# Kernel tuning notes

Measured on AMD Instinct MI355X. Metric: run time of the kernel, lower is better.

Reference implementation:

```python
import jax, jax.numpy as jnp
import numpy as np

V = 32000; DM = 1024; DS = 16; NL = 2; DC = 4; EXP = 2
DI = EXP * DM          # 2048 inner dim
DTR = DM // 16         # 64 dt_rank = ceil(d_model/16)
B = 2; L = 1024


def setup_inputs() -> dict:
    key = jax.random.key(0)
    ks = jax.random.split(key, 9)
    s = lambda k, shp, sc: jax.random.normal(k, shp, jnp.float32) * sc
    return {
        "input_ids": jax.random.randint(ks[0], (B, L), 0, V),
        "embed": s(ks[1], (V, DM), 0.02),
        "in_proj": s(ks[2], (NL, DM, 2 * DI), DM ** -0.5),
        "conv_w": s(ks[3], (NL, DI, DC), 0.2),
        "conv_b": jnp.zeros((NL, DI), jnp.float32),
        "x_proj": s(ks[4], (NL, DI, DTR + 2 * DS), DI ** -0.5),
        "dt_proj_w": s(ks[5], (NL, DTR, DI), DTR ** -0.5),
        "dt_proj_b": jnp.full((NL, DI), -4.6, jnp.float32),  # softplus ~= 0.01
        "A_log": jnp.tile(jnp.log(jnp.arange(1, DS + 1, dtype=jnp.float32))[None, None, :], (NL, DI, 1)),
        "D": jnp.ones((NL, DI), jnp.float32),
        "out_proj": s(ks[6], (NL, DI, DM), DI ** -0.5),
        "ln_g": jnp.ones((DM,), jnp.float32),
        "ln_b": jnp.zeros((DM,), jnp.float32),
        "head": s(ks[7], (DM, V), DM ** -0.5),
    }


def _silu(x):
    return x * jax.nn.sigmoid(x)


def _mamba_layer(x, Wi, cw, cb, Wx, Wdt, bdt, A_log, Dv, Wo):
    # x: [B,L,DM]
    xz = x @ Wi                                   # [B,L,2*DI]
    xin, z = jnp.split(xz, 2, axis=-1)
    # causal depthwise conv1d, kernel DC
    xp = jnp.pad(xin, ((0, 0), (DC - 1, 0), (0, 0)))
    conv = sum(xp[:, k:k + x.shape[1], :] * cw[:, k] for k in range(DC)) + cb
    u = _silu(conv)                               # [B,L,DI]
    dbc = u @ Wx                                  # [B,L,DTR+2*DS]
    dt = dbc[..., :DTR]
    Bm = dbc[..., DTR:DTR + DS]                   # [B,L,DS]
    Cm = dbc[..., DTR + DS:]                      # [B,L,DS]
    delta = jax.nn.softplus(dt @ Wdt + bdt)       # [B,L,DI]
    A = -jnp.exp(A_log)                           # [DI,DS]
    dA = jnp.exp(delta[..., None] * A)            # [B,L,DI,DS]
    dBu = (delta * u)[..., None] * Bm[:, :, None, :]

    def comb(c1, c2):
        a1, b1 = c1
        a2, b2 = c2
        return a1 * a2, a2 * b1 + b2

    _, h = jax.lax.associative_scan(comb, (dA, dBu), axis=1)  # [B,L,DI,DS]
    y = jnp.einsum('bldn,bln->bld', h, Cm) + u * Dv
    y = y * _silu(z)
    return y @ Wo


def reference(input_ids, embed, in_proj, conv_w, conv_b, x_proj, dt_proj_w,
              dt_proj_b, A_log, D, out_proj, ln_g, ln_b, head):
    x = embed[input_ids]                          # [B,L,DM]
    for i in range(NL):
        x = _mamba_layer(x, in_proj[i], conv_w[i], conv_b[i], x_proj[i],
                         dt_proj_w[i], dt_proj_b[i], A_log[i], D[i], out_proj[i])
    mu = jnp.mean(x, -1, keepdims=True)
    var = jnp.var(x, -1, keepdims=True)
    x = (x - mu) * jax.lax.rsqrt(var + 1e-5) * ln_g + ln_b
    return x @ head                               # [B,L,V]
```

## Files before the change

kernel.cpp:

```cpp
#include <hip/hip_runtime.h>

typedef unsigned short u16;
typedef __attribute__((ext_vector_type(8))) short bf16x8;
typedef __attribute__((ext_vector_type(4))) float f32x4;
typedef __attribute__((ext_vector_type(4))) u16 u16x4;

#define DEV static __device__ __forceinline__

DEV u16 f2bf(float f) {
  union { float f; unsigned u; } v; v.f = f;
  unsigned r = (v.u + 0x7fffu + ((v.u >> 16) & 1u)) >> 16;
  return (u16)r;
}

DEV void gload_lds16(const void* g, void* l) {
  __builtin_amdgcn_global_load_lds(
      (const __attribute__((address_space(1))) unsigned int*)g,
      (__attribute__((address_space(3))) unsigned int*)l, 16, 0, 0);
}

#define STGH(buf, mat, half, P, kt) { \
    const int r_ = (half) * 128 + sr0; \
    gload_lds16((P) + (size_t)r_ * K + (kt) + scs, &lds[buf][mat][r_][sc8]); \
    gload_lds16((P) + (size_t)(r_ + 64) * K + (kt) + scs, &lds[buf][mat][r_ + 64][sc8]); }
#define LDB(buf) _Pragma("unroll") for (int n = 0; n < 4; ++n) { \
    const int row = wn * 64 + n * 16 + lr; \
    _Pragma("unroll") for (int kk = 0; kk < 2; ++kk) \
      bfr[n][kk] = *(const bf16x8*)&lds[buf][1][row][(((kk << 2) | lq) ^ (row & 7)) << 3]; }
#define LDA(buf, p) _Pragma("unroll") for (int mi = 0; mi < 2; ++mi) { \
    const int row = wm * 128 + ((p) * 2 + mi) * 16 + lr; \
    _Pragma("unroll") for (int kk = 0; kk < 2; ++kk) \
      af[mi][kk] = *(const bf16x8*)&lds[buf][0][row][(((kk << 2) | lq) ^ (row & 7)) << 3]; }
#define MM(p) __builtin_amdgcn_s_setprio(1); \
  _Pragma("unroll") for (int kk = 0; kk < 2; ++kk) \
  _Pragma("unroll") for (int mi = 0; mi < 2; ++mi) \
  _Pragma("unroll") for (int n = 0; n < 4; ++n) \
    acc[(p) * 2 + mi][n] = __builtin_amdgcn_mfma_f32_16x16x32_bf16(af[mi][kk], bfr[n][kk], acc[(p) * 2 + mi][n], 0, 0, 0); \
  __builtin_amdgcn_s_setprio(0);
#define BAR() { __builtin_amdgcn_s_barrier(); asm volatile("" ::: "memory"); }
#define WLG() { asm volatile("s_waitcnt lgkmcnt(0)" ::: "memory"); __builtin_amdgcn_sched_barrier(0); }
#define VMC(n) asm volatile("s_waitcnt vmcnt(" #n ")" ::: "memory")

__global__ __launch_bounds__(512, 1)
void gemm256(const u16* __restrict__ A, const u16* __restrict__ BT,
             float* __restrict__ C, int M, int N, int K) {
  __shared__ u16 lds[2][2][256][64];
  const int t = threadIdx.x;
  const int l = t & 63;
  const int w = t >> 6;
  const int wm = w >> 2;
  const int wn = w & 3;
  const int lr = l & 15, lq = l >> 4;

  const int gn = N >> 8;
  const int nwg = gn << 3;
  const int orig = blockIdx.y * 8 + blockIdx.x;
  const int q = nwg >> 3;
  const int swz = (orig & 7) * q + (orig >> 3);
  const int bx = swz & 7;
  const int by = swz >> 3;

  const u16* Ap = A + (size_t)bx * 256 * K;
  const u16* Bp = BT + (size_t)by * 256 * K;
  const int sr0 = t >> 3;
  const int sc8 = (t & 7) << 3;
  const int scs = (((t & 7) ^ (sr0 & 7)) << 3);

  f32x4 acc[8][4];
#pragma unroll
  for (int m = 0; m < 8; ++m)
#pragma unroll
    for (int n = 0; n < 4; ++n) acc[m][n] = (f32x4){0.f, 0.f, 0.f, 0.f};

  const int NI = K >> 7;
  STGH(0, 1, 0, Bp, 0) STGH(0, 1, 1, Bp, 0)
  STGH(0, 0, 0, Ap, 0) STGH(0, 0, 1, Ap, 0)
  STGH(1, 1, 0, Bp, 64) STGH(1, 1, 1, Bp, 64)
  VMC(4);
  BAR();

  for (int ip = 0; ip < NI; ++ip) {
    const int k0 = ip << 7;
    const bool m2 = (k0 + 128) < K;
    const bool m3 = (k0 + 192) < K;
    bf16x8 bfr[4][2], af[2][2];
    LDB(0) LDA(0, 0)
    STGH(1, 0, 0, Ap, k0 + 64)
    BAR(); WLG(); MM(0) BAR();
    LDA(0, 1)
    STGH(1, 0, 1, Ap, k0 + 64)
    BAR(); WLG(); MM(1) BAR();
    LDA(0, 2)
    if (m2) STGH(0, 1, 0, Bp, k0 + 128)
    BAR(); WLG(); MM(2) BAR();
    LDA(0, 3)
    if (m2) STGH(0, 1, 1, Bp, k0 + 128)
    BAR(); WLG(); MM(3)
    if (m2) { VMC(4); } else { VMC(0); }
    BAR();
    LDB(1) LDA(1, 0)
    if (m2) STGH(0, 0, 0, Ap, k0 + 128)
    BAR(); WLG(); MM(0) BAR();
    LDA(1, 1)
    if (m2) STGH(0, 0, 1, Ap, k0 + 128)
    BAR(); WLG(); MM(1) BAR();
    LDA(1, 2)
    if (m3) STGH(1, 1, 0, Bp, k0 + 192)
    BAR(); WLG(); MM(2) BAR();
    LDA(1, 3)
    if (m3) STGH(1, 1, 1, Bp, k0 + 192)
    BAR(); WLG(); MM(3)
    if (m3) { VMC(4); } else { VMC(0); }
    BAR();
  }

  const int lg4 = lq * 4;
#pragma unroll
  for (int m = 0; m < 8; ++m) {
    const int grow0 = bx * 256 + wm * 128 + m * 16 + lg4;
#pragma unroll
    for (int n = 0; n < 4; ++n) {
      const int gcol = by * 256 + wn * 64 + n * 16 + lr;
#pragma unroll
      for (int r = 0; r < 4; ++r) {
        const size_t idx = (size_t)(grow0 + r) * N + gcol;
        C[idx] = acc[m][n][r];
      }
    }
  }
}
#undef STGH
#undef LDB
#undef LDA
#undef MM
#undef BAR
#undef WLG
#undef VMC

template<int EPI>
__global__ __launch_bounds__(256)
void gemm_bt(const u16* __restrict__ A, const u16* __restrict__ BT,
             float* __restrict__ C, const float* __restrict__ bias,
             int M, int N, int K) {
  __shared__ u16 As[128][64];
  __shared__ u16 Bs[128][64];
  const int t = threadIdx.x;
  const int l = t & 63;
  const int w = t >> 6;
  const int wr = (w >> 1) * 64;
  const int wc = (w & 1) * 64;

  const int nwg = gridDim.x * gridDim.y;
  const int orig = blockIdx.y * gridDim.x + blockIdx.x;
  const int swz = (orig & 7) * (nwg >> 3) + (orig >> 3);
  const int bx = swz & 15;
  const int by = swz >> 4;

  const size_t aoff = (size_t)bx * 128 * K;
  const size_t boff = (size_t)by * 128 * K;
  const int r0 = t >> 3;
  const int c0s = (((t & 7) ^ (r0 & 7)) << 3);
  const int c0l = (t & 7) << 3;
  const int lr = l & 15;
  const int lq = l >> 4;

  f32x4 acc[4][4];
#pragma unroll
  for (int i = 0; i < 4; ++i)
#pragma unroll
    for (int j = 0; j < 4; ++j) acc[i][j] = (f32x4){0.f, 0.f, 0.f, 0.f};

  for (int kt = 0; kt < K; kt += 64) {
    __syncthreads();
#pragma unroll
    for (int i = 0; i < 4; ++i) {
      const int r = r0 + i * 32;
      gload_lds16(A + aoff + (size_t)r * K + kt + c0s, &As[r][c0l]);
      gload_lds16(BT + boff + (size_t)r * K + kt + c0s, &Bs[r][c0l]);
    }
    __syncthreads();
#pragma unroll
    for (int kk = 0; kk < 2; ++kk) {
      bf16x8 af[4], bfr[4];
#pragma unroll
      for (int i = 0; i < 4; ++i) {
        const int row = wr + i * 16 + lr;
        af[i] = *(const bf16x8*)&As[row][(((kk << 2) | lq) ^ (row & 7)) << 3];
      }
#pragma unroll
      for (int j = 0; j < 4; ++j) {
        const int row = wc + j * 16 + lr;
        bfr[j] = *(const bf16x8*)&Bs[row][(((kk << 2) | lq) ^ (row & 7)) << 3];
      }
#pragma unroll
      for (int i = 0; i < 4; ++i)
#pragma unroll
        for (int j = 0; j < 4; ++j)
          acc[i][j] = __builtin_amdgcn_mfma_f32_16x16x32_bf16(af[i], bfr[j], acc[i][j], 0, 0, 0);
    }
  }

  const int lg4 = lq * 4;
#pragma unroll
  for (int i = 0; i < 4; ++i) {
    const int grow0 = bx * 128 + wr + i * 16 + lg4;
#pragma unroll
    for (int j = 0; j < 4; ++j) {
      const int gcol = by * 128 + wc + j * 16 + lr;
      float bv = 0.f;
      if (EPI == 1) bv = bias[gcol];
#pragma unroll
      for (int r = 0; r < 4; ++r) {
        float v = acc[i][j][r];
        if (EPI == 1) {
          v += bv;
          v = fmaxf(v, 0.f) + log1pf(expf(-fabsf(v)));
        }
        C[(size_t)(grow0 + r) * N + gcol] = v;
      }
    }
  }
}

__global__ __launch_bounds__(256)
void xproj_split(const u16* __restrict__ A, const u16* __restrict__ BT,
                 float* __restrict__ P) {
  __shared__ u16 As[128][64];
  __shared__ u16 Bs[128][64];
  const int t = threadIdx.x;
  const int l = t & 63;
  const int w = t >> 6;
  const int wr = (w >> 1) * 64;
  const int wc = (w & 1) * 64;
  const int bx = blockIdx.x;
  const int ch = blockIdx.y;
  const int kb = ch * 256;

  const size_t aoff = (size_t)bx * 128 * 2048 + kb;
  const int r0 = t >> 3;
  const int c0s = (((t & 7) ^ (r0 & 7)) << 3);
  const int c0l = (t & 7) << 3;
  const int lr = l & 15;
  const int lq = l >> 4;

  f32x4 acc[4][4];
#pragma unroll
  for (int i = 0; i < 4; ++i)
#pragma unroll
    for (int j = 0; j < 4; ++j) acc[i][j] = (f32x4){0.f, 0.f, 0.f, 0.f};

  for (int kt = 0; kt < 256; kt += 64) {
    __syncthreads();
#pragma unroll
    for (int i = 0; i < 4; ++i) {
      const int r = r0 + i * 32;
      gload_lds16(A + aoff + (size_t)r * 2048 + kt + c0s, &As[r][c0l]);
      gload_lds16(BT + (size_t)r * 2048 + kb + kt + c0s, &Bs[r][c0l]);
    }
    __syncthreads();
#pragma unroll
    for (int kk = 0; kk < 2; ++kk) {
      bf16x8 af[4], bfr[4];
#pragma unroll
      for (int i = 0; i < 4; ++i) {
        const int row = wr + i * 16 + lr;
        af[i] = *(const bf16x8*)&As[row][(((kk << 2) | lq) ^ (row & 7)) << 3];
      }
#pragma unroll
      for (int j = 0; j < 4; ++j) {
        const int row = wc + j * 16 + lr;
        bfr[j] = *(const bf16x8*)&Bs[row][(((kk << 2) | lq) ^ (row & 7)) << 3];
      }
#pragma unroll
      for (int i = 0; i < 4; ++i)
#pragma unroll
        for (int j = 0; j < 4; ++j)
          acc[i][j] = __builtin_amdgcn_mfma_f32_16x16x32_bf16(af[i], bfr[j], acc[i][j], 0, 0, 0);
    }
  }

  float* __restrict__ Pc = P + (size_t)ch * 262144;
  const int lg4 = lq * 4;
#pragma unroll
  for (int i = 0; i < 4; ++i) {
    const int grow0 = bx * 128 + wr + i * 16 + lg4;
#pragma unroll
    for (int j = 0; j < 4; ++j) {
      const int gcol = wc + j * 16 + lr;
#pragma unroll
      for (int r = 0; r < 4; ++r)
        Pc[(size_t)(grow0 + r) * 128 + gcol] = acc[i][j][r];
    }
  }
}

__global__ __launch_bounds__(256)
void merge_x(const float* __restrict__ P, float* __restrict__ dbc,
             u16* __restrict__ dtbf) {
  const int idx = blockIdx.x * 256 + threadIdx.x;
  float s = 0.f;
#pragma unroll
  for (int ch = 0; ch < 8; ++ch) s += P[(size_t)ch * 262144 + idx];
  dbc[idx] = s;
  const int c = idx & 127, r = idx >> 7;
  if (c < 64) dtbf[r * 64 + c] = f2bf(s);
}

__global__ __launch_bounds__(256)
void outproj_split(const u16* __restrict__ A, const u16* __restrict__ BT,
                   float* __restrict__ P) {
  __shared__ u16 As[128][64];
  __shared__ u16 Bs[128][64];
  const int t = threadIdx.x;
  const int l = t & 63;
  const int w = t >> 6;
  const int wr = (w >> 1) * 64;
  const int wc = (w & 1) * 64;
  const int bx = blockIdx.x;
  const int byn = blockIdx.y & 7;
  const int ch = blockIdx.y >> 3;
  const int kb = ch * 1024;

  const size_t aoff = (size_t)bx * 128 * 2048 + kb;
  const size_t boff = (size_t)byn * 128 * 2048 + kb;
  const int r0 = t >> 3;
  const int c0s = (((t & 7) ^ (r0 & 7)) << 3);
  const int c0l = (t & 7) << 3;
  const int lr = l & 15;
  const int lq = l >> 4;

  f32x4 acc[4][4];
#pragma unroll
  for (int i = 0; i < 4; ++i)
#pragma unroll
    for (int j = 0; j < 4; ++j) acc[i][j] = (f32x4){0.f, 0.f, 0.f, 0.f};

  for (int kt = 0; kt < 1024; kt += 64) {
    __syncthreads();
#pragma unroll
    for (int i = 0; i < 4; ++i) {
      const int r = r0 + i * 32;
      gload_lds16(A + aoff + (size_t)r * 2048 + kt + c0s, &As[r][c0l]);
      gload_lds16(BT + boff + (size_t)r * 2048 + kt + c0s, &Bs[r][c0l]);
    }
    __syncthreads();
#pragma unroll
    for (int kk = 0; kk < 2; ++kk) {
      bf16x8 af[4], bfr[4];
#pragma unroll
      for (int i = 0; i < 4; ++i) {
        const int row = wr + i * 16 + lr;
        af[i] = *(const bf16x8*)&As[row][(((kk << 2) | lq) ^ (row & 7)) << 3];
      }
#pragma unroll
      for (int j = 0; j < 4; ++j) {
        const int row = wc + j * 16 + lr;
        bfr[j] = *(const bf16x8*)&Bs[row][(((kk << 2) | lq) ^ (row & 7)) << 3];
      }
#pragma unroll
      for (int i = 0; i < 4; ++i)
#pragma unroll
        for (int j = 0; j < 4; ++j)
          acc[i][j] = __builtin_amdgcn_mfma_f32_16x16x32_bf16(af[i], bfr[j], acc[i][j], 0, 0, 0);
    }
  }

  float* __restrict__ Pc = P + (size_t)ch * 2097152;
  const int lg4 = lq * 4;
#pragma unroll
  for (int i = 0; i < 4; ++i) {
    const int grow0 = bx * 128 + wr + i * 16 + lg4;
#pragma unroll
    for (int j = 0; j < 4; ++j) {
      const int gcol = byn * 128 + wc + j * 16 + lr;
#pragma unroll
      for (int r = 0; r < 4; ++r)
        Pc[(size_t)(grow0 + r) * 1024 + gcol] = acc[i][j][r];
    }
  }
}

__global__ __launch_bounds__(256)
void merge_o1(const float* __restrict__ P, u16* __restrict__ xbf) {
  const int i4 = (blockIdx.x * 256 + threadIdx.x) * 4;
  const float4 a = *(const float4*)(P + i4);
  const float4 b = *(const float4*)(P + 2097152 + i4);
  u16x4 o = { f2bf(a.x + b.x), f2bf(a.y + b.y), f2bf(a.z + b.z), f2bf(a.w + b.w) };
  *(u16x4*)(xbf + i4) = o;
}

__global__ __launch_bounds__(256)
void merge_o2_ln(const float* __restrict__ P, const float* __restrict__ g,
                 const float* __restrict__ bta, u16* __restrict__ out) {
  __shared__ float red1[4], red2[4];
  const int r = blockIdx.x;
  const int tid = threadIdx.x;
  const int lane = tid & 63, wid = tid >> 6;
  const int c4 = tid * 4;
  const float4 a = *(const float4*)(P + (size_t)r * 1024 + c4);
  const float4 b = *(const float4*)(P + 2097152 + (size_t)r * 1024 + c4);
  float4 v = { a.x + b.x, a.y + b.y, a.z + b.z, a.w + b.w };
  float s = v.x + v.y + v.z + v.w;
#pragma unroll
  for (int m = 1; m < 64; m <<= 1) s += __shfl_xor(s, m, 64);
  if (lane == 0) red1[wid] = s;
  __syncthreads();
  const float mu = (red1[0] + red1[1] + red1[2] + red1[3]) * (1.f / 1024.f);
  const float d0 = v.x - mu, d1 = v.y - mu, d2 = v.z - mu, d3 = v.w - mu;
  float q = d0 * d0 + d1 * d1 + d2 * d2 + d3 * d3;
#pragma unroll
  for (int m = 1; m < 64; m <<= 1) q += __shfl_xor(q, m, 64);
  if (lane == 0) red2[wid] = q;
  __syncthreads();
  const float rs = rsqrtf((red2[0] + red2[1] + red2[2] + red2[3]) * (1.f / 1024.f) + 1e-5f);
  const float4 gv = *(const float4*)(g + c4);
  const float4 bv = *(const float4*)(bta + c4);
  u16x4 o = { f2bf(d0 * rs * gv.x + bv.x), f2bf(d1 * rs * gv.y + bv.y),
              f2bf(d2 * rs * gv.z + bv.z), f2bf(d3 * rs * gv.w + bv.w) };
  *(u16x4*)(out + (size_t)r * 1024 + c4) = o;
}

struct TBatch {
  const float* src[10];
  u16* dst[10];
  int K[10], N[10], tx[10];
  int start[11];
  int njobs;
  const int* ids;
};

__global__ __launch_bounds__(256)
void transpose_batch(TBatch tb) {
  const int tile = blockIdx.x;
  int j = 0;
  while (j + 1 < tb.njobs && tile >= tb.start[j + 1]) ++j;
  const int lt = tile - tb.start[j];

  if (tb.tx[j] < 0) {
    const int c = threadIdx.x * 4;
    const int id = tb.ids[lt];
    const float4 v = *(const float4*)(tb.src[j] + (size_t)id * 1024 + c);
    u16x4 o = { f2bf(v.x), f2bf(v.y), f2bf(v.z), f2bf(v.w) };
    *(u16x4*)(tb.dst[j] + (size_t)lt * 1024 + c) = o;
    return;
  }

  const int K = tb.K[j];
  const int N = tb.N[j];
  const int kb = (lt % tb.tx[j]) * 32;
  const int nb = (lt / tb.tx[j]) * 32;
  const float* __restrict__ in = tb.src[j];
  u16* __restrict__ out = tb.dst[j];

  __shared__ float tile_s[32][33];
  const int tx = threadIdx.x & 31;
  const int ty = threadIdx.x >> 5;
#pragma unroll
  for (int s = 0; s < 4; ++s) {
    const int k = kb + ty + s * 8;
    const int n = nb + tx;
    tile_s[ty + s * 8][tx] = (n < N) ? __builtin_nontemporal_load(in + (size_t)k * N + n) : 0.f;
  }
  __syncthreads();
#pragma unroll
  for (int s = 0; s < 4; ++s) {
    const int n = nb + ty + s * 8;
    const int k = kb + tx;
    out[(size_t)n * K + k] = f2bf(tile_s[tx][ty + s * 8]);
  }
}

__global__ __launch_bounds__(256)
void conv_silu4(const float* __restrict__ xz, const float* __restrict__ cw,
                const float* __restrict__ cb, float* __restrict__ u,
                u16* __restrict__ ubf) {
  const int i4 = (blockIdx.x * 256 + threadIdx.x) * 4;
  const int d = i4 & 2047;
  const int r = i4 >> 11;
  const int t = r & 1023;
  float4 acc = *(const float4*)(cb + d);
  const float4 w0 = *(const float4*)(cw + (d + 0) * 4);
  const float4 w1 = *(const float4*)(cw + (d + 1) * 4);
  const float4 w2 = *(const float4*)(cw + (d + 2) * 4);
  const float4 w3 = *(const float4*)(cw + (d + 3) * 4);
#pragma unroll
  for (int k = 0; k < 4; ++k) {
    const int tt = t - 3 + k;
    if (tt >= 0) {
      const float4 x4 = *(const float4*)(xz + (size_t)(r - 3 + k) * 4096 + d);
      acc.x = fmaf(x4.x, ((const float*)&w0)[k], acc.x);
      acc.y = fmaf(x4.y, ((const float*)&w1)[k], acc.y);
      acc.z = fmaf(x4.z, ((const float*)&w2)[k], acc.z);
      acc.w = fmaf(x4.w, ((const float*)&w3)[k], acc.w);
    }
  }
  const float4 s = { acc.x / (1.f + __expf(-acc.x)), acc.y / (1.f + __expf(-acc.y)),
                     acc.z / (1.f + __expf(-acc.z)), acc.w / (1.f + __expf(-acc.w)) };
  *(float4*)(u + i4) = s;
  u16x4 o = { f2bf(s.x), f2bf(s.y), f2bf(s.z), f2bf(s.w) };
  *(u16x4*)(ubf + i4) = o;
}

__global__ __launch_bounds__(256)
void scan_pass1(const float* __restrict__ delta, const float* __restrict__ u,
                const float* __restrict__ dbc, const float* __restrict__ A_log,
                float* __restrict__ Pb, float* __restrict__ Qb) {
  const int blk = blockIdx.x;
  const int ch = blk & 15;
  if (ch == 15) return;
  const int dt = (blk >> 4) & 7;
  const int b = blk >> 7;
  const int d = dt * 256 + threadIdx.x;

  float Ac[16], h[16], P[16];
#pragma unroll
  for (int n = 0; n < 16; ++n) {
    Ac[n] = -expf(A_log[d * 16 + n]) * 1.44269504f;
    h[n] = 0.f;
    P[n] = 1.f;
  }
  const int r0 = b * 1024 + ch * 64;
  for (int j = 0; j < 64; ++j) {
    const size_t r = r0 + j;
    const float dlt = delta[r * 2048 + d];
    const float uu = u[r * 2048 + d];
    const float du = dlt * uu;
    const float4 B0 = *(const float4*)(dbc + r * 128 + 64);
    const float4 B1 = *(const float4*)(dbc + r * 128 + 68);
    const float4 B2 = *(const float4*)(dbc + r * 128 + 72);
    const float4 B3 = *(const float4*)(dbc + r * 128 + 76);
    const float Bv[16] = { B0.x, B0.y, B0.z, B0.w, B1.x, B1.y, B1.z, B1.w,
                           B2.x, B2.y, B2.z, B2.w, B3.x, B3.y, B3.z, B3.w };
#pragma unroll
    for (int n = 0; n < 16; ++n) {
      const float da = exp2f(dlt * Ac[n]);
      P[n] *= da;
      h[n] = fmaf(da, h[n], du * Bv[n]);
    }
  }
  const size_t o = ((size_t)ch * 4096 + b * 2048 + d) * 16;
#pragma unroll
  for (int n = 0; n < 16; ++n) { Pb[o + n] = P[n]; Qb[o + n] = h[n]; }
}

__global__ __launch_bounds__(256)
void scan_pass2(const float* __restrict__ delta, const float* __restrict__ u,
                const float* __restrict__ dbc, const float* __restrict__ xz,
                const float* __restrict__ A_log, const float* __restrict__ Dp,
                const float* __restrict__ Pb, const float* __restrict__ Qb,
                u16* __restrict__ ybf) {
  const int blk = blockIdx.x;
  const int ch = blk & 15;
  const int dt = (blk >> 4) & 7;
  const int b = blk >> 7;
  const int d = dt * 256 + threadIdx.x;

  float Ac[16], h[16];
#pragma unroll
  for (int n = 0; n < 16; ++n) {
    Ac[n] = -expf(A_log[d * 16 + n]) * 1.44269504f;
    h[n] = 0.f;
  }
  const float Dd = Dp[d];

  for (int cc = 0; cc < ch; ++cc) {
    const size_t o = ((size_t)cc * 4096 + b * 2048 + d) * 16;
#pragma unroll
    for (int n = 0; n < 16; ++n)
      h[n] = fmaf(Pb[o + n], h[n], Qb[o + n]);
  }

  const int r0 = b * 1024 + ch * 64;
  for (int j = 0; j < 64; ++j) {
    const size_t r = r0 + j;
    const float dlt = delta[r * 2048 + d];
    const float uu = u[r * 2048 + d];
    const float zz = xz[r * 4096 + 2048 + d];
    const float du = dlt * uu;
    const float4 B0 = *(const float4*)(dbc + r * 128 + 64);
    const float4 B1 = *(const float4*)(dbc + r * 128 + 68);
    const float4 B2 = *(const float4*)(dbc + r * 128 + 72);
    const float4 B3 = *(const float4*)(dbc + r * 128 + 76);
    const float4 C0 = *(const float4*)(dbc + r * 128 + 80);
    const float4 C1 = *(const float4*)(dbc + r * 128 + 84);
    const float4 C2 = *(const float4*)(dbc + r * 128 + 88);
    const float4 C3 = *(const float4*)(dbc + r * 128 + 92);
    const float Bv[16] = { B0.x, B0.y, B0.z, B0.w, B1.x, B1.y, B1.z, B1.w,
                           B2.x, B2.y, B2.z, B2.w, B3.x, B3.y, B3.z, B3.w };
    const float Cv[16] = { C0.x, C0.y, C0.z, C0.w, C1.x, C1.y, C1.z, C1.w,
                           C2.x, C2.y, C2.z, C2.w, C3.x, C3.y, C3.z, C3.w };
    float p0 = 0.f, p1 = 0.f, p2 = 0.f, p3 = 0.f;
#pragma unroll
    for (int n = 0; n < 16; n += 4) {
      float da;
      da = exp2f(dlt * Ac[n + 0]); h[n + 0] = fmaf(da, h[n + 0], du * Bv[n + 0]); p0 = fmaf(h[n + 0], Cv[n + 0], p0);
      da = exp2f(dlt * Ac[n + 1]); h[n + 1] = fmaf(da, h[n + 1], du * Bv[n + 1]); p1 = fmaf(h[n + 1], Cv[n + 1], p1);
      da = exp2f(dlt * Ac[n + 2]); h[n + 2] = fmaf(da, h[n + 2], du * Bv[n + 2]); p2 = fmaf(h[n + 2], Cv[n + 2], p2);
      da = exp2f(dlt * Ac[n + 3]); h[n + 3] = fmaf(da, h[n + 3], du * Bv[n + 3]); p3 = fmaf(h[n + 3], Cv[n + 3], p3);
    }
    const float p = (p0 + p1) + (p2 + p3);
    const float yv = (p + uu * Dd) * (zz / (1.f + __expf(-zz)));
    ybf[r * 2048 + d] = f2bf(yv);
  }
}

extern "C" void kernel_launch(void* const* d_in, const int* in_sizes, int n_in,
                              void* d_out, int out_size, void* d_ws, size_t ws_size,
                              hipStream_t stream) {
  (void)in_sizes; (void)n_in; (void)out_size; (void)ws_size;
  const int*   ids      = (const int*)d_in[0];
  const float* embed    = (const float*)d_in[1];
  const float* in_proj  = (const float*)d_in[2];
  const float* conv_w   = (const float*)d_in[3];
  const float* conv_b   = (const float*)d_in[4];
  const float* x_proj   = (const float*)d_in[5];
  const float* dt_w     = (const float*)d_in[6];
  const float* dt_b     = (const float*)d_in[7];
  const float* A_log    = (const float*)d_in[8];
  const float* Dp       = (const float*)d_in[9];
  const float* out_proj = (const float*)d_in[10];
  const float* ln_g     = (const float*)d_in[11];
  const float* ln_bta   = (const float*)d_in[12];
  const float* head     = (const float*)d_in[13];

  float* fout = (float*)d_out;
  float* xz   = fout;
  float* ubuf = fout + 8388608;
  float* dbuf = fout + 12582912;
  float* dbc  = fout + 16777216;
  float* Pb   = fout + 17039360;
  float* Qb   = fout + 18087936;
  float* xpp  = fout + 19136512;
  float* opp  = fout + 21233664;

  u16* tail = (u16*)(fout + 26000000);
  u16* WiT[2]  = { tail,                tail + 4194304 };
  u16* WxT[2]  = { tail + 8388608,      tail + 8650752 };
  u16* WdtT[2] = { tail + 8912896,      tail + 9043968 };
  u16* WoT[2]  = { tail + 9175040,      tail + 11272192 };

  char* wp = (char*)d_ws;
  u16* headT = (u16*)wp; wp += (size_t)32000 * 1024 * 2;
  u16* xbf   = (u16*)wp; wp += (size_t)2048 * 1024 * 2;
  u16* ubf   = (u16*)wp; wp += (size_t)2048 * 2048 * 2;
  u16* dtbf  = (u16*)wp; wp += (size_t)2048 * 64 * 2;
  u16* ybf   = (u16*)wp; wp += (size_t)2048 * 2048 * 2;
  u16* xlnbf = (u16*)wp; wp += (size_t)2048 * 1024 * 2;

  const dim3 tb(256);
  const dim3 tb5(512);

  TBatch t{};
  int nj = 0, acc = 0;
  t.ids = ids;
  t.src[nj] = head; t.dst[nj] = headT;
  t.K[nj] = 1024; t.N[nj] = 32000; t.tx[nj] = 32;
  t.start[nj] = acc; acc += 32 * 1000; ++nj;
  for (int i = 0; i < 2; ++i) {
    t.src[nj] = in_proj + (size_t)i * 1024 * 4096; t.dst[nj] = WiT[i];
    t.K[nj] = 1024; t.N[nj] = 4096; t.tx[nj] = 32;
    t.start[nj] = acc; acc += 32 * 128; ++nj;
    t.src[nj] = x_proj + (size_t)i * 2048 * 96; t.dst[nj] = WxT[i];
    t.K[nj] = 2048; t.N[nj] = 96; t.tx[nj] = 64;
    t.start[nj] = acc; acc += 64 * 4; ++nj;
    t.src[nj] = dt_w + (size_t)i * 64 * 2048; t.dst[nj] = WdtT[i];
    t.K[nj] = 64; t.N[nj] = 2048; t.tx[nj] = 2;
    t.start[nj] = acc; acc += 2 * 64; ++nj;
    t.src[nj] = out_proj + (size_t)i * 2048 * 1024; t.dst[nj] = WoT[i];
    t.K[nj] = 2048; t.N[nj] = 1024; t.tx[nj] = 64;
    t.start[nj] = acc; acc += 64 * 32; ++nj;
  }
  t.src[nj] = embed; t.dst[nj] = xbf;
  t.K[nj] = 0; t.N[nj] = 0; t.tx[nj] = -1;
  t.start[nj] = acc; acc += 2048; ++nj;
  t.start[nj] = acc;
  t.njobs = nj;
  transpose_batch<<<acc, tb, 0, stream>>>(t);

  for (int i = 0; i < 2; ++i) {
    gemm_bt<0><<<dim3(16, 32), tb, 0, stream>>>(xbf, WiT[i], xz, nullptr, 2048, 4096, 1024);
    conv_silu4<<<4096, tb, 0, stream>>>(xz, conv_w + i * 2048 * 4, conv_b + i * 2048, ubuf, ubf);
    xproj_split<<<dim3(16, 8), tb, 0, stream>>>(ubf, WxT[i], xpp);
    merge_x<<<1024, tb, 0, stream>>>(xpp, dbc, dtbf);
    gemm_bt<1><<<dim3(16, 16), tb, 0, stream>>>(dtbf, WdtT[i], dbuf, dt_b + i * 2048, 2048, 2048, 64);
    scan_pass1<<<256, tb, 0, stream>>>(dbuf, ubuf, dbc, A_log + i * 2048 * 16, Pb, Qb);
    scan_pass2<<<256, tb, 0, stream>>>(dbuf, ubuf, dbc, xz, A_log + i * 2048 * 16, Dp + i * 2048, Pb, Qb, ybf);
    outproj_split<<<dim3(16, 16), tb, 0, stream>>>(ybf, WoT[i], opp);
    if (i == 0) {
      merge_o1<<<2048, tb, 0, stream>>>(opp, xbf);
    } else {
      merge_o2_ln<<<2048, tb, 0, stream>>>(opp, ln_g, ln_bta, xlnbf);
    }
  }

  gemm256<<<dim3(8, 125), tb5, 0, stream>>>(xlnbf, headT, fout, 2048, 32000, 1024);
}
```

Before: 606.1 us.

## Store delta and u as bf16, reuse bf16 u in scan, widen transpose tiles

```diff
diff --git a/kernel.cpp b/kernel.cpp
--- a/kernel.cpp
+++ b/kernel.cpp
@@ -4,6 +4,7 @@
 typedef __attribute__((ext_vector_type(8))) short bf16x8;
 typedef __attribute__((ext_vector_type(4))) float f32x4;
 typedef __attribute__((ext_vector_type(4))) u16 u16x4;
+typedef __attribute__((ext_vector_type(8))) u16 u16x8;
 
 #define DEV static __device__ __forceinline__
 
@@ -12,6 +13,8 @@
   unsigned r = (v.u + 0x7fffu + ((v.u >> 16) & 1u)) >> 16;
   return (u16)r;
 }
+
+DEV float bf2f(u16 v) { return __int_as_float(((int)v) << 16); }
 
 DEV void gload_lds16(const void* g, void* l) {
   __builtin_amdgcn_global_load_lds(
@@ -140,8 +143,8 @@
 template<int EPI>
 __global__ __launch_bounds__(256)
 void gemm_bt(const u16* __restrict__ A, const u16* __restrict__ BT,
-             float* __restrict__ C, const float* __restrict__ bias,
-             int M, int N, int K) {
+             float* __restrict__ C, u16* __restrict__ Cbf,
+             const float* __restrict__ bias, int M, int N, int K) {
   __shared__ u16 As[128][64];
   __shared__ u16 Bs[128][64];
   const int t = threadIdx.x;
@@ -212,11 +215,13 @@
 #pragma unroll
       for (int r = 0; r < 4; ++r) {
         float v = acc[i][j][r];
-        if (EPI == 1) {
+        if (EPI == 0) {
+          C[(size_t)(grow0 + r) * N + gcol] = v;
+        } else {
           v += bv;
           v = fmaxf(v, 0.f) + log1pf(expf(-fabsf(v)));
+          Cbf[(size_t)(grow0 + r) * N + gcol] = f2bf(v);
         }
-        C[(size_t)(grow0 + r) * N + gcol] = v;
       }
     }
   }
@@ -447,33 +452,40 @@
 
   const int K = tb.K[j];
   const int N = tb.N[j];
-  const int kb = (lt % tb.tx[j]) * 32;
-  const int nb = (lt / tb.tx[j]) * 32;
+  const int kb = (lt % tb.tx[j]) * 64;
+  const int nb = (lt / tb.tx[j]) * 64;
   const float* __restrict__ in = tb.src[j];
   u16* __restrict__ out = tb.dst[j];
 
-  __shared__ float tile_s[32][33];
-  const int tx = threadIdx.x & 31;
-  const int ty = threadIdx.x >> 5;
+  __shared__ float ts[64][65];
+  const int kl = threadIdx.x >> 2;
+  const int n16 = (threadIdx.x & 3) * 16;
+  const float* rowp = in + (size_t)(kb + kl) * N;
 #pragma unroll
   for (int s = 0; s < 4; ++s) {
-    const int k = kb + ty + s * 8;
-    const int n = nb + tx;
-    tile_s[ty + s * 8][tx] = (n < N) ? __builtin_nontemporal_load(in + (size_t)k * N + n) : 0.f;
+    const int n = nb + n16 + s * 4;
+    f32x4 v = { 0.f, 0.f, 0.f, 0.f };
+    if (n < N) v = __builtin_nontemporal_load((const f32x4*)(rowp + n));
+    ts[kl][n16 + s * 4 + 0] = v[0];
+    ts[kl][n16 + s * 4 + 1] = v[1];
+    ts[kl][n16 + s * 4 + 2] = v[2];
+    ts[kl][n16 + s * 4 + 3] = v[3];
   }
   __syncthreads();
-#pragma unroll
-  for (int s = 0; s < 4; ++s) {
-    const int n = nb + ty + s * 8;
-    const int k = kb + tx;
-    out[(size_t)n * K + k] = f2bf(tile_s[tx][ty + s * 8]);
+  const int k8 = (threadIdx.x & 7) * 8;
+#pragma unroll
+  for (int s = 0; s < 2; ++s) {
+    const int nl = (threadIdx.x >> 3) + s * 32;
+    u16x8 o;
+#pragma unroll
+    for (int i = 0; i < 8; ++i) o[i] = f2bf(ts[k8 + i][nl]);
+    *(u16x8*)(out + (size_t)(nb + nl) * K + kb + k8) = o;
   }
 }
 
 __global__ __launch_bounds__(256)
 void conv_silu4(const float* __restrict__ xz, const float* __restrict__ cw,
-                const float* __restrict__ cb, float* __restrict__ u,
-                u16* __restrict__ ubf) {
+                const float* __restrict__ cb, u16* __restrict__ ubf) {
   const int i4 = (blockIdx.x * 256 + threadIdx.x) * 4;
   const int d = i4 & 2047;
   const int r = i4 >> 11;
@@ -494,15 +506,13 @@
       acc.w = fmaf(x4.w, ((const float*)&w3)[k], acc.w);
     }
   }
-  const float4 s = { acc.x / (1.f + __expf(-acc.x)), acc.y / (1.f + __expf(-acc.y)),
-                     acc.z / (1.f + __expf(-acc.z)), acc.w / (1.f + __expf(-acc.w)) };
-  *(float4*)(u + i4) = s;
-  u16x4 o = { f2bf(s.x), f2bf(s.y), f2bf(s.z), f2bf(s.w) };
+  u16x4 o = { f2bf(acc.x / (1.f + __expf(-acc.x))), f2bf(acc.y / (1.f + __expf(-acc.y))),
+              f2bf(acc.z / (1.f + __expf(-acc.z))), f2bf(acc.w / (1.f + __expf(-acc.w))) };
   *(u16x4*)(ubf + i4) = o;
 }
 
 __global__ __launch_bounds__(256)
-void scan_pass1(const float* __restrict__ delta, const float* __restrict__ u,
+void scan_pass1(const u16* __restrict__ deltab, const u16* __restrict__ ub,
                 const float* __restrict__ dbc, const float* __restrict__ A_log,
                 float* __restrict__ Pb, float* __restrict__ Qb) {
   const int blk = blockIdx.x;
@@ -522,8 +532,8 @@
   const int r0 = b * 1024 + ch * 64;
   for (int j = 0; j < 64; ++j) {
     const size_t r = r0 + j;
-    const float dlt = delta[r * 2048 + d];
-    const float uu = u[r * 2048 + d];
+    const float dlt = bf2f(deltab[r * 2048 + d]);
+    const float uu = bf2f(ub[r * 2048 + d]);
     const float du = dlt * uu;
     const float4 B0 = *(const float4*)(dbc + r * 128 + 64);
     const float4 B1 = *(const float4*)(dbc + r * 128 + 68);
@@ -544,7 +554,7 @@
 }
 
 __global__ __launch_bounds__(256)
-void scan_pass2(const float* __restrict__ delta, const float* __restrict__ u,
+void scan_pass2(const u16* __restrict__ deltab, const u16* __restrict__ ub,
                 const float* __restrict__ dbc, const float* __restrict__ xz,
                 const float* __restrict__ A_log, const float* __restrict__ Dp,
                 const float* __restrict__ Pb, const float* __restrict__ Qb,
@@ -573,8 +583,8 @@
   const int r0 = b * 1024 + ch * 64;
   for (int j = 0; j < 64; ++j) {
     const size_t r = r0 + j;
-    const float dlt = delta[r * 2048 + d];
-    const float uu = u[r * 2048 + d];
+    const float dlt = bf2f(deltab[r * 2048 + d]);
+    const float uu = bf2f(ub[r * 2048 + d]);
     const float zz = xz[r * 4096 + 2048 + d];
     const float du = dlt * uu;
     const float4 B0 = *(const float4*)(dbc + r * 128 + 64);
@@ -625,8 +635,6 @@
 
   float* fout = (float*)d_out;
   float* xz   = fout;
-  float* ubuf = fout + 8388608;
-  float* dbuf = fout + 12582912;
   float* dbc  = fout + 16777216;
   float* Pb   = fout + 17039360;
   float* Qb   = fout + 18087936;
@@ -638,6 +646,7 @@
   u16* WxT[2]  = { tail + 8388608,      tail + 8650752 };
   u16* WdtT[2] = { tail + 8912896,      tail + 9043968 };
   u16* WoT[2]  = { tail + 9175040,      tail + 11272192 };
+  u16* dbf     = tail + 13369344;
 
   char* wp = (char*)d_ws;
   u16* headT = (u16*)wp; wp += (size_t)32000 * 1024 * 2;
@@ -654,21 +663,21 @@
   int nj = 0, acc = 0;
   t.ids = ids;
   t.src[nj] = head; t.dst[nj] = headT;
-  t.K[nj] = 1024; t.N[nj] = 32000; t.tx[nj] = 32;
-  t.start[nj] = acc; acc += 32 * 1000; ++nj;
+  t.K[nj] = 1024; t.N[nj] = 32000; t.tx[nj] = 16;
+  t.start[nj] = acc; acc += 16 * 500; ++nj;
   for (int i = 0; i < 2; ++i) {
     t.src[nj] = in_proj + (size_t)i * 1024 * 4096; t.dst[nj] = WiT[i];
-    t.K[nj] = 1024; t.N[nj] = 4096; t.tx[nj] = 32;
-    t.start[nj] = acc; acc += 32 * 128; ++nj;
+    t.K[nj] = 1024; t.N[nj] = 4096; t.tx[nj] = 16;
+    t.start[nj] = acc; acc += 16 * 64; ++nj;
     t.src[nj] = x_proj + (size_t)i * 2048 * 96; t.dst[nj] = WxT[i];
-    t.K[nj] = 2048; t.N[nj] = 96; t.tx[nj] = 64;
-    t.start[nj] = acc; acc += 64 * 4; ++nj;
+    t.K[nj] = 2048; t.N[nj] = 96; t.tx[nj] = 32;
+    t.start[nj] = acc; acc += 32 * 2; ++nj;
     t.src[nj] = dt_w + (size_t)i * 64 * 2048; t.dst[nj] = WdtT[i];
-    t.K[nj] = 64; t.N[nj] = 2048; t.tx[nj] = 2;
-    t.start[nj] = acc; acc += 2 * 64; ++nj;
+    t.K[nj] = 64; t.N[nj] = 2048; t.tx[nj] = 1;
+    t.start[nj] = acc; acc += 1 * 32; ++nj;
     t.src[nj] = out_proj + (size_t)i * 2048 * 1024; t.dst[nj] = WoT[i];
-    t.K[nj] = 2048; t.N[nj] = 1024; t.tx[nj] = 64;
-    t.start[nj] = acc; acc += 64 * 32; ++nj;
+    t.K[nj] = 2048; t.N[nj] = 1024; t.tx[nj] = 32;
+    t.start[nj] = acc; acc += 32 * 16; ++nj;
   }
   t.src[nj] = embed; t.dst[nj] = xbf;
   t.K[nj] = 0; t.N[nj] = 0; t.tx[nj] = -1;
@@ -678,13 +687,13 @@
   transpose_batch<<<acc, tb, 0, stream>>>(t);
 
   for (int i = 0; i < 2; ++i) {
-    gemm_bt<0><<<dim3(16, 32), tb, 0, stream>>>(xbf, WiT[i], xz, nullptr, 2048, 4096, 1024);
-    conv_silu4<<<4096, tb, 0, stream>>>(xz, conv_w + i * 2048 * 4, conv_b + i * 2048, ubuf, ubf);
+    gemm_bt<0><<<dim3(16, 32), tb, 0, stream>>>(xbf, WiT[i], xz, nullptr, nullptr, 2048, 4096, 1024);
+    conv_silu4<<<4096, tb, 0, stream>>>(xz, conv_w + i * 2048 * 4, conv_b + i * 2048, ubf);
     xproj_split<<<dim3(16, 8), tb, 0, stream>>>(ubf, WxT[i], xpp);
     merge_x<<<1024, tb, 0, stream>>>(xpp, dbc, dtbf);
-    gemm_bt<1><<<dim3(16, 16), tb, 0, stream>>>(dtbf, WdtT[i], dbuf, dt_b + i * 2048, 2048, 2048, 64);
-    scan_pass1<<<256, tb, 0, stream>>>(dbuf, ubuf, dbc, A_log + i * 2048 * 16, Pb, Qb);
-    scan_pass2<<<256, tb, 0, stream>>>(dbuf, ubuf, dbc, xz, A_log + i * 2048 * 16, Dp + i * 2048, Pb, Qb, ybf);
+    gemm_bt<1><<<dim3(16, 16), tb, 0, stream>>>(dtbf, WdtT[i], nullptr, dbf, dt_b + i * 2048, 2048, 2048, 64);
+    scan_pass1<<<256, tb, 0, stream>>>(dbf, ubf, dbc, A_log + i * 2048 * 16, Pb, Qb);
+    scan_pass2<<<256, tb, 0, stream>>>(dbf, ubf, dbc, xz, A_log + i * 2048 * 16, Dp + i * 2048, Pb, Qb, ybf);
     outproj_split<<<dim3(16, 16), tb, 0, stream>>>(ybf, WoT[i], opp);
     if (i == 0) {
       merge_o1<<<2048, tb, 0, stream>>>(opp, xbf);
```

Result: slower. 665.7 us (+9.8%).
